# Performance work log

Measured on AMD Instinct MI355X. Metric: run time of the kernel, lower is better.

The kernel has to match this reference:

```python
import jax, jax.numpy as jnp
import numpy as np

# Problem sizes (see shape_source): N points, D embedding dim, B subbatches (events), M labels per event.
N, D, B, M = 2_097_152, 16, 8, 32
DELTA_V, DELTA_D = 0.5, 1.5  # module defaults
EPS = 1e-8


def setup_inputs() -> dict:
    key = jax.random.key(0)
    outputs = jax.random.normal(key, (N, D), dtype=jnp.float32)
    idx = jnp.arange(N)
    # contiguous subbatches, every label present in every subbatch (matches torch.unique structure)
    subbatch_indices = (idx // (N // B)).astype(jnp.int32)
    labels = (idx % M).astype(jnp.int32)
    return {"outputs": outputs, "labels": labels, "subbatch_indices": subbatch_indices}


def reference(outputs, labels, subbatch_indices):
    # normalize=True: L2-normalize each embedding row (note: torch adds eps to the norm, not norm+eps clamp)
    x = outputs / (jnp.linalg.norm(outputs, axis=1) + EPS)[:, None]

    # flat segment id per (subbatch, label) group; every group is populated by construction
    seg = (subbatch_indices * M + labels).astype(jnp.int32)  # [N] in [0, B*M)

    ones = jnp.ones((x.shape[0],), x.dtype)
    counts = jax.ops.segment_sum(ones, seg, num_segments=B * M)        # [B*M] == Nm per group
    mus = jax.ops.segment_sum(x, seg, num_segments=B * M) / counts[:, None]  # [B*M, D] centroids

    # L_pull: per-point hinge on L1 distance to its centroid, weights are all-ones (use_weights=False)
    dist = jnp.sum(jnp.abs(mus[seg] - x), axis=1)                       # [N] L1 distance
    L_pull = jnp.sum(jax.nn.relu(dist - DELTA_V) ** 2 / (M * counts[seg]))

    # L_push: all-pairs centroid hinge within each subbatch, diagonal zeroed
    mus_b = mus.reshape(B, M, D)
    pd = jnp.sum(jnp.abs(mus_b[:, :, None, :] - mus_b[:, None, :, :]), axis=-1)  # [B, M, M]
    hinge = jax.nn.relu(2.0 * DELTA_D - pd) ** 2
    hinge = jnp.where(jnp.eye(M, dtype=bool)[None], 0.0, hinge)
    L_push = jnp.sum(hinge) / (M * (M - 1))

    return (L_pull + L_push) / B
```

## Files before the change

kernel.cpp:

```cpp
#include <hip/hip_runtime.h>
#include <math.h>


#define DD 16
#define MM 32
#define BBATCH 8
#define SEGS 256
#define DELTA_V 0.5f
#define DELTA_D 1.5f
#define NEPS 1e-8f

#define NTHR 256
#define TILE_PTS 256
#define TPB 8
#define CHUNK_PTS (TILE_PTS * TPB)
#define DEPTH 2
#define KP 32
#define MAXBLK 2048

#define OFF_PP    0
#define OFF_MUS   (KP * 4352)
#define OFF_INVW  (OFF_MUS + 4096)
#define OFF_PUSH  (OFF_INVW + 256)
#define OFF_PULL  (OFF_PUSH + 16)
#define WS_ZERO_FLOATS (KP * 4352)

__device__ __forceinline__ void gload16(const void* g, void* l) {
    __builtin_amdgcn_global_load_lds(
        (const __attribute__((address_space(1))) void*)g,
        (__attribute__((address_space(3))) void*)l, 16, 0, 0);
}
__device__ __forceinline__ void gload4(const void* g, void* l) {
    __builtin_amdgcn_global_load_lds(
        (const __attribute__((address_space(1))) void*)g,
        (__attribute__((address_space(3))) void*)l, 4, 0, 0);
}

__device__ __forceinline__ void lds_fadd(float* p, float v) {
    __hip_atomic_fetch_add(p, v, __ATOMIC_RELAXED, __HIP_MEMORY_SCOPE_WORKGROUP);
}

__device__ __forceinline__ float block_reduce_sum(float v) {
    #pragma unroll
    for (int o = 32; o > 0; o >>= 1) v += __shfl_down(v, o, 64);
    __shared__ float red[4];
    int wid  = threadIdx.x >> 6;
    int lane = threadIdx.x & 63;
    if (lane == 0) red[wid] = v;
    __syncthreads();
    v = (threadIdx.x < (NTHR >> 6)) ? red[threadIdx.x] : 0.0f;
    if (wid == 0) {
        #pragma unroll
        for (int o = 32; o > 0; o >>= 1) v += __shfl_down(v, o, 64);
    }
    return v;
}

__device__ __forceinline__ void flush_point(float* lsT, int seg,
                                            float4 a0, float4 a1,
                                            float4 a2, float4 a3, float cnt) {
    lds_fadd(&lsT[ 0*SEGS + seg], a0.x); lds_fadd(&lsT[ 1*SEGS + seg], a0.y);
    lds_fadd(&lsT[ 2*SEGS + seg], a0.z); lds_fadd(&lsT[ 3*SEGS + seg], a0.w);
    lds_fadd(&lsT[ 4*SEGS + seg], a1.x); lds_fadd(&lsT[ 5*SEGS + seg], a1.y);
    lds_fadd(&lsT[ 6*SEGS + seg], a1.z); lds_fadd(&lsT[ 7*SEGS + seg], a1.w);
    lds_fadd(&lsT[ 8*SEGS + seg], a2.x); lds_fadd(&lsT[ 9*SEGS + seg], a2.y);
    lds_fadd(&lsT[10*SEGS + seg], a2.z); lds_fadd(&lsT[11*SEGS + seg], a2.w);
    lds_fadd(&lsT[12*SEGS + seg], a3.x); lds_fadd(&lsT[13*SEGS + seg], a3.y);
    lds_fadd(&lsT[14*SEGS + seg], a3.z); lds_fadd(&lsT[15*SEGS + seg], a3.w);
    lds_fadd(&lsT[16*SEGS + seg], cnt);
}

#define STAGE_TILE(bi_, pb_) do {                                              \
    const float* gs_ = (const float*)o4 + (size_t)(pb_) * DD;                  \
    { int q_ = (w << 8) +   0 + lane;                                          \
      gload16(gs_ + (q_ ^ ((q_ >> 3) & 3)) * 4, &dbuf[bi_][((w << 8) +   0) * 4]); } \
    { int q_ = (w << 8) +  64 + lane;                                          \
      gload16(gs_ + (q_ ^ ((q_ >> 3) & 3)) * 4, &dbuf[bi_][((w << 8) +  64) * 4]); } \
    { int q_ = (w << 8) + 128 + lane;                                          \
      gload16(gs_ + (q_ ^ ((q_ >> 3) & 3)) * 4, &dbuf[bi_][((w << 8) + 128) * 4]); } \
    { int q_ = (w << 8) + 192 + lane;                                          \
      gload16(gs_ + (q_ ^ ((q_ >> 3) & 3)) * 4, &dbuf[bi_][((w << 8) + 192) * 4]); } \
    gload4(labels + (pb_) + (w << 6) + lane, &labbuf[bi_][w << 6]);            \
    gload4(sub    + (pb_) + (w << 6) + lane, &subbuf[bi_][w << 6]);            \
} while (0)

__global__ void __launch_bounds__(NTHR)
k_segsum(const float4* __restrict__ o4,
         const int* __restrict__ labels,
         const int* __restrict__ sub,
         float* __restrict__ pp,
         int n) {
    __shared__ float lsT[(DD + 1) * SEGS];
    __shared__ float dbuf[DEPTH][TILE_PTS * DD];
    __shared__ int   labbuf[DEPTH][TILE_PTS];
    __shared__ int   subbuf[DEPTH][TILE_PTS];
    for (int i = threadIdx.x; i < (DD + 1) * SEGS; i += NTHR) lsT[i] = 0.0f;
    __syncthreads();

    const int t    = threadIdx.x;
    const int w    = t >> 6;
    const int lane = t & 63;
    const int xm   = (t >> 1) & 3;

    float4 c0 = {0,0,0,0}, c1 = {0,0,0,0}, c2 = {0,0,0,0}, c3 = {0,0,0,0};
    float cnt = 0.0f;
    int cur = -1;

    const int nchunks = n / CHUNK_PTS;
    for (int cb = blockIdx.x; cb < nchunks; cb += gridDim.x) {
        const int pbase = cb * CHUNK_PTS;
        STAGE_TILE(0, pbase + 0 * TILE_PTS);
        STAGE_TILE(1, pbase + 1 * TILE_PTS);
        #pragma unroll
        for (int ti = 0; ti < TPB; ++ti) {
            const int bi = ti & 1;
            if (ti < TPB - 1) asm volatile("s_waitcnt vmcnt(6)" ::: "memory");
            else              asm volatile("s_waitcnt vmcnt(0)" ::: "memory");
            int lb = labbuf[bi][t];
            int sv = subbuf[bi][t];
            const float* db = &dbuf[bi][0];
            float4 a = *(const float4*)&db[((4*t + 0) ^ xm) * 4];
            float4 b = *(const float4*)&db[((4*t + 1) ^ xm) * 4];
            float4 c = *(const float4*)&db[((4*t + 2) ^ xm) * 4];
            float4 e = *(const float4*)&db[((4*t + 3) ^ xm) * 4];
            int seg = sv * MM + lb;
            float ss = a.x*a.x + a.y*a.y + a.z*a.z + a.w*a.w
                     + b.x*b.x + b.y*b.y + b.z*b.z + b.w*b.w
                     + c.x*c.x + c.y*c.y + c.z*c.z + c.w*c.w
                     + e.x*e.x + e.y*e.y + e.z*e.z + e.w*e.w;
            float rn = 1.0f / (sqrtf(ss) + NEPS);
            if (seg != cur) {
                if (cur >= 0) flush_point(lsT, cur, c0, c1, c2, c3, cnt);
                c0 = c1 = c2 = c3 = (float4){0,0,0,0};
                cnt = 0.0f;
                cur = seg;
            }
            c0.x = fmaf(a.x, rn, c0.x); c0.y = fmaf(a.y, rn, c0.y);
            c0.z = fmaf(a.z, rn, c0.z); c0.w = fmaf(a.w, rn, c0.w);
            c1.x = fmaf(b.x, rn, c1.x); c1.y = fmaf(b.y, rn, c1.y);
            c1.z = fmaf(b.z, rn, c1.z); c1.w = fmaf(b.w, rn, c1.w);
            c2.x = fmaf(c.x, rn, c2.x); c2.y = fmaf(c.y, rn, c2.y);
            c2.z = fmaf(c.z, rn, c2.z); c2.w = fmaf(c.w, rn, c2.w);
            c3.x = fmaf(e.x, rn, c3.x); c3.y = fmaf(e.y, rn, c3.y);
            c3.z = fmaf(e.z, rn, c3.z); c3.w = fmaf(e.w, rn, c3.w);
            cnt += 1.0f;
            __builtin_amdgcn_sched_barrier(0);
            if (ti + 2 < TPB) STAGE_TILE(bi, pbase + (ti + 2) * TILE_PTS);
        }
    }
    if (blockIdx.x == 0) {
        for (int p = nchunks * CHUNK_PTS + t; p < n; p += NTHR) {
            float4 a = o4[4*p+0], b = o4[4*p+1], c = o4[4*p+2], e = o4[4*p+3];
            int seg = sub[p] * MM + labels[p];
            float ss = a.x*a.x + a.y*a.y + a.z*a.z + a.w*a.w
                     + b.x*b.x + b.y*b.y + b.z*b.z + b.w*b.w
                     + c.x*c.x + c.y*c.y + c.z*c.z + c.w*c.w
                     + e.x*e.x + e.y*e.y + e.z*e.z + e.w*e.w;
            float rn = 1.0f / (sqrtf(ss) + NEPS);
            if (seg != cur) {
                if (cur >= 0) flush_point(lsT, cur, c0, c1, c2, c3, cnt);
                c0 = c1 = c2 = c3 = (float4){0,0,0,0};
                cnt = 0.0f;
                cur = seg;
            }
            c0.x = fmaf(a.x, rn, c0.x); c0.y = fmaf(a.y, rn, c0.y);
            c0.z = fmaf(a.z, rn, c0.z); c0.w = fmaf(a.w, rn, c0.w);
            c1.x = fmaf(b.x, rn, c1.x); c1.y = fmaf(b.y, rn, c1.y);
            c1.z = fmaf(b.z, rn, c1.z); c1.w = fmaf(b.w, rn, c1.w);
            c2.x = fmaf(c.x, rn, c2.x); c2.y = fmaf(c.y, rn, c2.y);
            c2.z = fmaf(c.z, rn, c2.z); c2.w = fmaf(c.w, rn, c2.w);
            c3.x = fmaf(e.x, rn, c3.x); c3.y = fmaf(e.y, rn, c3.y);
            c3.z = fmaf(e.z, rn, c3.z); c3.w = fmaf(e.w, rn, c3.w);
            cnt += 1.0f;
        }
    }
    if (cur >= 0) flush_point(lsT, cur, c0, c1, c2, c3, cnt);
    __syncthreads();

    float* dst = pp + (size_t)(blockIdx.x & (KP - 1)) * (SEGS * 17);
    for (int s = threadIdx.x; s < SEGS; s += NTHR) {
        float c = lsT[DD * SEGS + s];
        if (c != 0.0f) {
            #pragma unroll
            for (int d = 0; d < DD; ++d)
                unsafeAtomicAdd(&dst[s * 17 + d], lsT[d * SEGS + s]);
            unsafeAtomicAdd(&dst[s * 17 + 16], c);
        }
    }
}

__global__ void k_finalize_push(float* __restrict__ ws) {
    const float* pp = ws + OFF_PP;
    float* mus  = ws + OFF_MUS;
    float* invw = ws + OFF_INVW;
    float* push = ws + OFF_PUSH;

    __shared__ float muT[DD * SEGS];
    int t = threadIdx.x;

    float s17[DD + 1];
    #pragma unroll
    for (int d = 0; d <= DD; ++d) s17[d] = 0.0f;
    for (int k = 0; k < KP; ++k) {
        const float* src = pp + (size_t)k * (SEGS * 17) + t * 17;
        #pragma unroll
        for (int d = 0; d <= DD; ++d) s17[d] += src[d];
    }
    float cnt = s17[DD];
    float ic  = (cnt > 0.0f) ? 1.0f / cnt : 0.0f;
    #pragma unroll
    for (int d = 0; d < DD; ++d) {
        float m = s17[d] * ic;
        mus[t * DD + d]   = m;
        muT[d * SEGS + t] = m;
    }
    invw[t] = (cnt > 0.0f) ? 1.0f / ((float)MM * cnt) : 0.0f;
    __syncthreads();

    int b = t >> 5, m1 = t & 31;
    float acc = 0.0f;
    for (int m2 = 0; m2 < MM; ++m2) {
        float pd = 0.0f;
        #pragma unroll
        for (int d = 0; d < DD; ++d)
            pd += fabsf(muT[d * SEGS + b * MM + m1] - muT[d * SEGS + b * MM + m2]);
        float h = 2.0f * DELTA_D - pd;
        if (m2 != m1 && h > 0.0f) acc += h * h;
    }
    float tot = block_reduce_sum(acc);
    if (t == 0) push[0] = tot / (float)(MM * (MM - 1));
}

__global__ void __launch_bounds__(NTHR)
k_pull(const float4* __restrict__ o4,
       const int* __restrict__ labels,
       const int* __restrict__ sub,
       const float* __restrict__ mus,
       const float* __restrict__ invw,
       float* __restrict__ pull_part,
       int n) {
    __shared__ float muL[DD * SEGS];
    __shared__ float siw[SEGS];
    __shared__ float dbuf[DEPTH][TILE_PTS * DD];
    __shared__ int   labbuf[DEPTH][TILE_PTS];
    __shared__ int   subbuf[DEPTH][TILE_PTS];
    for (int i = threadIdx.x; i < DD * SEGS; i += NTHR) muL[i] = mus[i];
    for (int i = threadIdx.x; i < SEGS; i += NTHR) siw[i] = invw[i];
    __syncthreads();

    const int t    = threadIdx.x;
    const int w    = t >> 6;
    const int lane = t & 63;
    const int xm   = (t >> 1) & 3;

    float4 m0, m1, m2, m3;
    float iw = 0.0f;
    int cur = -1;
    float acc = 0.0f;

    const int nchunks = n / CHUNK_PTS;
    for (int cb = blockIdx.x; cb < nchunks; cb += gridDim.x) {
        const int pbase = cb * CHUNK_PTS;
        STAGE_TILE(0, pbase + 0 * TILE_PTS);
        STAGE_TILE(1, pbase + 1 * TILE_PTS);
        #pragma unroll
        for (int ti = 0; ti < TPB; ++ti) {
            const int bi = ti & 1;
            if (ti < TPB - 1) asm volatile("s_waitcnt vmcnt(6)" ::: "memory");
            else              asm volatile("s_waitcnt vmcnt(0)" ::: "memory");
            int lb = labbuf[bi][t];
            int sv = subbuf[bi][t];
            const float* db = &dbuf[bi][0];
            float4 a = *(const float4*)&db[((4*t + 0) ^ xm) * 4];
            float4 b = *(const float4*)&db[((4*t + 1) ^ xm) * 4];
            float4 c = *(const float4*)&db[((4*t + 2) ^ xm) * 4];
            float4 e = *(const float4*)&db[((4*t + 3) ^ xm) * 4];
            int seg = sv * MM + lb;
            if (seg != cur) {
                cur = seg;
                m0 = *(const float4*)&muL[seg * DD +  0];
                m1 = *(const float4*)&muL[seg * DD +  4];
                m2 = *(const float4*)&muL[seg * DD +  8];
                m3 = *(const float4*)&muL[seg * DD + 12];
                iw = siw[seg];
            }
            float ss = a.x*a.x + a.y*a.y + a.z*a.z + a.w*a.w
                     + b.x*b.x + b.y*b.y + b.z*b.z + b.w*b.w
                     + c.x*c.x + c.y*c.y + c.z*c.z + c.w*c.w
                     + e.x*e.x + e.y*e.y + e.z*e.z + e.w*e.w;
            float rn = 1.0f / (sqrtf(ss) + NEPS);
            float dist;
            dist  = fabsf(m0.x - a.x * rn) + fabsf(m0.y - a.y * rn)
                  + fabsf(m0.z - a.z * rn) + fabsf(m0.w - a.w * rn);
            dist += fabsf(m1.x - b.x * rn) + fabsf(m1.y - b.y * rn)
                  + fabsf(m1.z - b.z * rn) + fabsf(m1.w - b.w * rn);
            dist += fabsf(m2.x - c.x * rn) + fabsf(m2.y - c.y * rn)
                  + fabsf(m2.z - c.z * rn) + fabsf(m2.w - c.w * rn);
            dist += fabsf(m3.x - e.x * rn) + fabsf(m3.y - e.y * rn)
                  + fabsf(m3.z - e.z * rn) + fabsf(m3.w - e.w * rn);
            float h = dist - DELTA_V;
            if (h > 0.0f) acc = fmaf(h * h, iw, acc);
            __builtin_amdgcn_sched_barrier(0);
            if (ti + 2 < TPB) STAGE_TILE(bi, pbase + (ti + 2) * TILE_PTS);
        }
    }
    if (blockIdx.x == 0) {
        for (int p = nchunks * CHUNK_PTS + t; p < n; p += NTHR) {
            float4 a = o4[4*p+0], b = o4[4*p+1], c = o4[4*p+2], e = o4[4*p+3];
            int seg = sub[p] * MM + labels[p];
            if (seg != cur) {
                cur = seg;
                m0 = *(const float4*)&muL[seg * DD +  0];
                m1 = *(const float4*)&muL[seg * DD +  4];
                m2 = *(const float4*)&muL[seg * DD +  8];
                m3 = *(const float4*)&muL[seg * DD + 12];
                iw = siw[seg];
            }
            float ss = a.x*a.x + a.y*a.y + a.z*a.z + a.w*a.w
                     + b.x*b.x + b.y*b.y + b.z*b.z + b.w*b.w
                     + c.x*c.x + c.y*c.y + c.z*c.z + c.w*c.w
                     + e.x*e.x + e.y*e.y + e.z*e.z + e.w*e.w;
            float rn = 1.0f / (sqrtf(ss) + NEPS);
            float dist;
            dist  = fabsf(m0.x - a.x * rn) + fabsf(m0.y - a.y * rn)
                  + fabsf(m0.z - a.z * rn) + fabsf(m0.w - a.w * rn);
            dist += fabsf(m1.x - b.x * rn) + fabsf(m1.y - b.y * rn)
                  + fabsf(m1.z - b.z * rn) + fabsf(m1.w - b.w * rn);
            dist += fabsf(m2.x - c.x * rn) + fabsf(m2.y - c.y * rn)
                  + fabsf(m2.z - c.z * rn) + fabsf(m2.w - c.w * rn);
            dist += fabsf(m3.x - e.x * rn) + fabsf(m3.y - e.y * rn)
                  + fabsf(m3.z - e.z * rn) + fabsf(m3.w - e.w * rn);
            float h = dist - DELTA_V;
            if (h > 0.0f) acc = fmaf(h * h, iw, acc);
        }
    }
    float tot = block_reduce_sum(acc);
    if (threadIdx.x == 0) pull_part[blockIdx.x] = tot;
}

__global__ void k_final(const float* __restrict__ ws, float* __restrict__ out,
                        int nblk) {
    const float* push      = ws + OFF_PUSH;
    const float* pull_part = ws + OFF_PULL;
    int t = threadIdx.x;
    float v = 0.0f;
    for (int k = t; k < nblk; k += NTHR) v += pull_part[k];
    float tot = block_reduce_sum(v);
    if (t == 0) out[0] = (tot + push[0]) * (1.0f / (float)BBATCH);
}

extern "C" void kernel_launch(void* const* d_in, const int* in_sizes, int n_in,
                              void* d_out, int out_size, void* d_ws, size_t ws_size,
                              hipStream_t stream) {
    const float* outputs = (const float*)d_in[0];
    const int* labels    = (const int*)d_in[1];
    const int* sub       = (const int*)d_in[2];
    int n = in_sizes[0] / DD;

    float* ws        = (float*)d_ws;
    float* pp        = ws + OFF_PP;
    float* mus       = ws + OFF_MUS;
    float* invw      = ws + OFF_INVW;
    float* pull_part = ws + OFF_PULL;

    int nchunks = n / CHUNK_PTS;
    int nblk = nchunks < 1 ? 1 : (nchunks > MAXBLK ? MAXBLK : nchunks);

    hipMemsetAsync(d_ws, 0, (size_t)WS_ZERO_FLOATS * sizeof(float), stream);

    k_segsum<<<nblk, NTHR, 0, stream>>>((const float4*)outputs, labels, sub,
                                        pp, n);
    k_finalize_push<<<1, NTHR, 0, stream>>>(ws);
    k_pull<<<nblk, NTHR, 0, stream>>>((const float4*)outputs, labels, sub,
                                      mus, invw, pull_part, n);
    k_final<<<1, NTHR, 0, stream>>>(ws, (float*)d_out, nblk);
}
```

Baseline: 299.4 us.

## Shrink LDS footprint by flushing segment sums to global atomics and reusing buffers

Removes the per-block LDS segment-sum table and centroid copy so both streaming kernels use only the staging buffers, targeting higher occupancy (launch bounds raised to 4 blocks). Mid-stream segment flushes now go straight to global atomics in a transposed partial layout. The tail flush reuses the staging buffer as the LDS table. k_pull reads centroids from global memory rather than LDS. Because labels change almost every point, this risks far more global atomic traffic and contention.

Result: slower. 383.5 us (+28.1%).

```diff
diff --git a/kernel.cpp b/kernel.cpp
--- a/kernel.cpp
+++ b/kernel.cpp
@@ -70,37 +70,51 @@
     lds_fadd(&lsT[16*SEGS + seg], cnt);
 }
 
+__device__ __forceinline__ void flush_global(float* dst, int seg,
+                                             float4 a0, float4 a1,
+                                             float4 a2, float4 a3, float cnt) {
+    unsafeAtomicAdd(&dst[ 0*SEGS + seg], a0.x); unsafeAtomicAdd(&dst[ 1*SEGS + seg], a0.y);
+    unsafeAtomicAdd(&dst[ 2*SEGS + seg], a0.z); unsafeAtomicAdd(&dst[ 3*SEGS + seg], a0.w);
+    unsafeAtomicAdd(&dst[ 4*SEGS + seg], a1.x); unsafeAtomicAdd(&dst[ 5*SEGS + seg], a1.y);
+    unsafeAtomicAdd(&dst[ 6*SEGS + seg], a1.z); unsafeAtomicAdd(&dst[ 7*SEGS + seg], a1.w);
+    unsafeAtomicAdd(&dst[ 8*SEGS + seg], a2.x); unsafeAtomicAdd(&dst[ 9*SEGS + seg], a2.y);
+    unsafeAtomicAdd(&dst[10*SEGS + seg], a2.z); unsafeAtomicAdd(&dst[11*SEGS + seg], a2.w);
+    unsafeAtomicAdd(&dst[12*SEGS + seg], a3.x); unsafeAtomicAdd(&dst[13*SEGS + seg], a3.y);
+    unsafeAtomicAdd(&dst[14*SEGS + seg], a3.z); unsafeAtomicAdd(&dst[15*SEGS + seg], a3.w);
+    unsafeAtomicAdd(&dst[16*SEGS + seg], cnt);
+}
+
 #define STAGE_TILE(bi_, pb_) do {                                              \
     const float* gs_ = (const float*)o4 + (size_t)(pb_) * DD;                  \
+    float* db_ = smem + (bi_) * (TILE_PTS * DD);                               \
     { int q_ = (w << 8) +   0 + lane;                                          \
-      gload16(gs_ + (q_ ^ ((q_ >> 3) & 3)) * 4, &dbuf[bi_][((w << 8) +   0) * 4]); } \
+      gload16(gs_ + (size_t)(q_ ^ ((q_ >> 3) & 3)) * 4, db_ + ((w << 8) +   0) * 4); } \
     { int q_ = (w << 8) +  64 + lane;                                          \
-      gload16(gs_ + (q_ ^ ((q_ >> 3) & 3)) * 4, &dbuf[bi_][((w << 8) +  64) * 4]); } \
+      gload16(gs_ + (size_t)(q_ ^ ((q_ >> 3) & 3)) * 4, db_ + ((w << 8) +  64) * 4); } \
     { int q_ = (w << 8) + 128 + lane;                                          \
-      gload16(gs_ + (q_ ^ ((q_ >> 3) & 3)) * 4, &dbuf[bi_][((w << 8) + 128) * 4]); } \
+      gload16(gs_ + (size_t)(q_ ^ ((q_ >> 3) & 3)) * 4, db_ + ((w << 8) + 128) * 4); } \
     { int q_ = (w << 8) + 192 + lane;                                          \
-      gload16(gs_ + (q_ ^ ((q_ >> 3) & 3)) * 4, &dbuf[bi_][((w << 8) + 192) * 4]); } \
+      gload16(gs_ + (size_t)(q_ ^ ((q_ >> 3) & 3)) * 4, db_ + ((w << 8) + 192) * 4); } \
     gload4(labels + (pb_) + (w << 6) + lane, &labbuf[bi_][w << 6]);            \
     gload4(sub    + (pb_) + (w << 6) + lane, &subbuf[bi_][w << 6]);            \
 } while (0)
 
-__global__ void __launch_bounds__(NTHR)
+__global__ void __launch_bounds__(NTHR, 4)
 k_segsum(const float4* __restrict__ o4,
          const int* __restrict__ labels,
          const int* __restrict__ sub,
          float* __restrict__ pp,
          int n) {
-    __shared__ float lsT[(DD + 1) * SEGS];
-    __shared__ float dbuf[DEPTH][TILE_PTS * DD];
+    __shared__ float smem[DEPTH * TILE_PTS * DD];
     __shared__ int   labbuf[DEPTH][TILE_PTS];
     __shared__ int   subbuf[DEPTH][TILE_PTS];
-    for (int i = threadIdx.x; i < (DD + 1) * SEGS; i += NTHR) lsT[i] = 0.0f;
-    __syncthreads();
 
     const int t    = threadIdx.x;
     const int w    = t >> 6;
     const int lane = t & 63;
     const int xm   = (t >> 1) & 3;
+
+    float* gdst = pp + (size_t)(blockIdx.x & (KP - 1)) * ((DD + 1) * SEGS);
 
     float4 c0 = {0,0,0,0}, c1 = {0,0,0,0}, c2 = {0,0,0,0}, c3 = {0,0,0,0};
     float cnt = 0.0f;
@@ -118,7 +132,7 @@
             else              asm volatile("s_waitcnt vmcnt(0)" ::: "memory");
             int lb = labbuf[bi][t];
             int sv = subbuf[bi][t];
-            const float* db = &dbuf[bi][0];
+            const float* db = smem + bi * (TILE_PTS * DD);
             float4 a = *(const float4*)&db[((4*t + 0) ^ xm) * 4];
             float4 b = *(const float4*)&db[((4*t + 1) ^ xm) * 4];
             float4 c = *(const float4*)&db[((4*t + 2) ^ xm) * 4];
@@ -130,7 +144,7 @@
                      + e.x*e.x + e.y*e.y + e.z*e.z + e.w*e.w;
             float rn = 1.0f / (sqrtf(ss) + NEPS);
             if (seg != cur) {
-                if (cur >= 0) flush_point(lsT, cur, c0, c1, c2, c3, cnt);
+                if (cur >= 0) flush_global(gdst, cur, c0, c1, c2, c3, cnt);
                 c0 = c1 = c2 = c3 = (float4){0,0,0,0};
                 cnt = 0.0f;
                 cur = seg;
@@ -158,7 +172,7 @@
                      + e.x*e.x + e.y*e.y + e.z*e.z + e.w*e.w;
             float rn = 1.0f / (sqrtf(ss) + NEPS);
             if (seg != cur) {
-                if (cur >= 0) flush_point(lsT, cur, c0, c1, c2, c3, cnt);
+                if (cur >= 0) flush_global(gdst, cur, c0, c1, c2, c3, cnt);
                 c0 = c1 = c2 = c3 = (float4){0,0,0,0};
                 cnt = 0.0f;
                 cur = seg;
@@ -174,17 +188,21 @@
             cnt += 1.0f;
         }
     }
+
+    __syncthreads();
+    float* lsT = smem;
+    for (int i = t; i < (DD + 1) * SEGS; i += NTHR) lsT[i] = 0.0f;
+    __syncthreads();
     if (cur >= 0) flush_point(lsT, cur, c0, c1, c2, c3, cnt);
     __syncthreads();
 
-    float* dst = pp + (size_t)(blockIdx.x & (KP - 1)) * (SEGS * 17);
-    for (int s = threadIdx.x; s < SEGS; s += NTHR) {
+    for (int s = t; s < SEGS; s += NTHR) {
         float c = lsT[DD * SEGS + s];
         if (c != 0.0f) {
             #pragma unroll
             for (int d = 0; d < DD; ++d)
-                unsafeAtomicAdd(&dst[s * 17 + d], lsT[d * SEGS + s]);
-            unsafeAtomicAdd(&dst[s * 17 + 16], c);
+                unsafeAtomicAdd(&gdst[d * SEGS + s], lsT[d * SEGS + s]);
+            unsafeAtomicAdd(&gdst[DD * SEGS + s], c);
         }
     }
 }
@@ -201,10 +219,11 @@
     float s17[DD + 1];
     #pragma unroll
     for (int d = 0; d <= DD; ++d) s17[d] = 0.0f;
+    #pragma unroll 2
     for (int k = 0; k < KP; ++k) {
-        const float* src = pp + (size_t)k * (SEGS * 17) + t * 17;
-        #pragma unroll
-        for (int d = 0; d <= DD; ++d) s17[d] += src[d];
+        const float* src = pp + (size_t)k * ((DD + 1) * SEGS) + t;
+        #pragma unroll
+        for (int d = 0; d <= DD; ++d) s17[d] += src[d * SEGS];
     }
     float cnt = s17[DD];
     float ic  = (cnt > 0.0f) ? 1.0f / cnt : 0.0f;
@@ -231,7 +250,7 @@
     if (t == 0) push[0] = tot / (float)(MM * (MM - 1));
 }
 
-__global__ void __launch_bounds__(NTHR)
+__global__ void __launch_bounds__(NTHR, 4)
 k_pull(const float4* __restrict__ o4,
        const int* __restrict__ labels,
        const int* __restrict__ sub,
@@ -239,14 +258,9 @@
        const float* __restrict__ invw,
        float* __restrict__ pull_part,
        int n) {
-    __shared__ float muL[DD * SEGS];
-    __shared__ float siw[SEGS];
-    __shared__ float dbuf[DEPTH][TILE_PTS * DD];
+    __shared__ float smem[DEPTH * TILE_PTS * DD];
     __shared__ int   labbuf[DEPTH][TILE_PTS];
     __shared__ int   subbuf[DEPTH][TILE_PTS];
-    for (int i = threadIdx.x; i < DD * SEGS; i += NTHR) muL[i] = mus[i];
-    for (int i = threadIdx.x; i < SEGS; i += NTHR) siw[i] = invw[i];
-    __syncthreads();
 
     const int t    = threadIdx.x;
     const int w    = t >> 6;
@@ -270,7 +284,7 @@
             else              asm volatile("s_waitcnt vmcnt(0)" ::: "memory");
             int lb = labbuf[bi][t];
             int sv = subbuf[bi][t];
-            const float* db = &dbuf[bi][0];
+            const float* db = smem + bi * (TILE_PTS * DD);
             float4 a = *(const float4*)&db[((4*t + 0) ^ xm) * 4];
             float4 b = *(const float4*)&db[((4*t + 1) ^ xm) * 4];
             float4 c = *(const float4*)&db[((4*t + 2) ^ xm) * 4];
@@ -278,11 +292,11 @@
             int seg = sv * MM + lb;
             if (seg != cur) {
                 cur = seg;
-                m0 = *(const float4*)&muL[seg * DD +  0];
-                m1 = *(const float4*)&muL[seg * DD +  4];
-                m2 = *(const float4*)&muL[seg * DD +  8];
-                m3 = *(const float4*)&muL[seg * DD + 12];
-                iw = siw[seg];
+                m0 = *(const float4*)&mus[seg * DD +  0];
+                m1 = *(const float4*)&mus[seg * DD +  4];
+                m2 = *(const float4*)&mus[seg * DD +  8];
+                m3 = *(const float4*)&mus[seg * DD + 12];
+                iw = invw[seg];
             }
             float ss = a.x*a.x + a.y*a.y + a.z*a.z + a.w*a.w
                      + b.x*b.x + b.y*b.y + b.z*b.z + b.w*b.w
@@ -310,11 +324,11 @@
             int seg = sub[p] * MM + labels[p];
             if (seg != cur) {
                 cur = seg;
-                m0 = *(const float4*)&muL[seg * DD +  0];
-                m1 = *(const float4*)&muL[seg * DD +  4];
-                m2 = *(const float4*)&muL[seg * DD +  8];
-                m3 = *(const float4*)&muL[seg * DD + 12];
-                iw = siw[seg];
+                m0 = *(const float4*)&mus[seg * DD +  0];
+                m1 = *(const float4*)&mus[seg * DD +  4];
+                m2 = *(const float4*)&mus[seg * DD +  8];
+                m3 = *(const float4*)&mus[seg * DD + 12];
+                iw = invw[seg];
             }
             float ss = a.x*a.x + a.y*a.y + a.z*a.z + a.w*a.w
                      + b.x*b.x + b.y*b.y + b.z*b.z + b.w*b.w
```

## Replace LDS-staged pull pass with direct grid-stride loads; transpose partial-sum layout

Applied to the files above, without the earlier changes.

The pull kernel no longer stages point tiles into LDS with async global-to-LDS loads and double buffering. Each thread now loads its own point's four float4 values straight from global memory in a grid-stride loop, with more blocks and a min-blocks launch bound of 6 to raise occupancy. The per-block partial centroid sums switch from a point-major stride of 17 to a dimension-major layout, so the global atomics and the finalize reads become coalesced. The trade-off is that the pull loads now rely on the hardware to hide latency and combine the strided per-thread accesses, rather than on explicit software pipelining.

New measurement: 272.1 us. 9.1% less time.

```diff
diff --git a/kernel.cpp b/kernel.cpp
--- a/kernel.cpp
+++ b/kernel.cpp
@@ -17,6 +17,7 @@
 #define DEPTH 2
 #define KP 32
 #define MAXBLK 2048
+#define PULLBLK 4096
 
 #define OFF_PP    0
 #define OFF_MUS   (KP * 4352)
@@ -73,13 +74,13 @@
 #define STAGE_TILE(bi_, pb_) do {                                              \
     const float* gs_ = (const float*)o4 + (size_t)(pb_) * DD;                  \
     { int q_ = (w << 8) +   0 + lane;                                          \
-      gload16(gs_ + (q_ ^ ((q_ >> 3) & 3)) * 4, &dbuf[bi_][((w << 8) +   0) * 4]); } \
+      gload16(gs_ + (size_t)(q_ ^ ((q_ >> 3) & 3)) * 4, &dbuf[bi_][((w << 8) +   0) * 4]); } \
     { int q_ = (w << 8) +  64 + lane;                                          \
-      gload16(gs_ + (q_ ^ ((q_ >> 3) & 3)) * 4, &dbuf[bi_][((w << 8) +  64) * 4]); } \
+      gload16(gs_ + (size_t)(q_ ^ ((q_ >> 3) & 3)) * 4, &dbuf[bi_][((w << 8) +  64) * 4]); } \
     { int q_ = (w << 8) + 128 + lane;                                          \
-      gload16(gs_ + (q_ ^ ((q_ >> 3) & 3)) * 4, &dbuf[bi_][((w << 8) + 128) * 4]); } \
+      gload16(gs_ + (size_t)(q_ ^ ((q_ >> 3) & 3)) * 4, &dbuf[bi_][((w << 8) + 128) * 4]); } \
     { int q_ = (w << 8) + 192 + lane;                                          \
-      gload16(gs_ + (q_ ^ ((q_ >> 3) & 3)) * 4, &dbuf[bi_][((w << 8) + 192) * 4]); } \
+      gload16(gs_ + (size_t)(q_ ^ ((q_ >> 3) & 3)) * 4, &dbuf[bi_][((w << 8) + 192) * 4]); } \
     gload4(labels + (pb_) + (w << 6) + lane, &labbuf[bi_][w << 6]);            \
     gload4(sub    + (pb_) + (w << 6) + lane, &subbuf[bi_][w << 6]);            \
 } while (0)
@@ -177,14 +178,14 @@
     if (cur >= 0) flush_point(lsT, cur, c0, c1, c2, c3, cnt);
     __syncthreads();
 
-    float* dst = pp + (size_t)(blockIdx.x & (KP - 1)) * (SEGS * 17);
-    for (int s = threadIdx.x; s < SEGS; s += NTHR) {
+    float* gdst = pp + (size_t)(blockIdx.x & (KP - 1)) * ((DD + 1) * SEGS);
+    for (int s = t; s < SEGS; s += NTHR) {
         float c = lsT[DD * SEGS + s];
         if (c != 0.0f) {
             #pragma unroll
             for (int d = 0; d < DD; ++d)
-                unsafeAtomicAdd(&dst[s * 17 + d], lsT[d * SEGS + s]);
-            unsafeAtomicAdd(&dst[s * 17 + 16], c);
+                unsafeAtomicAdd(&gdst[d * SEGS + s], lsT[d * SEGS + s]);
+            unsafeAtomicAdd(&gdst[DD * SEGS + s], c);
         }
     }
 }
@@ -201,10 +202,11 @@
     float s17[DD + 1];
     #pragma unroll
     for (int d = 0; d <= DD; ++d) s17[d] = 0.0f;
+    #pragma unroll 2
     for (int k = 0; k < KP; ++k) {
-        const float* src = pp + (size_t)k * (SEGS * 17) + t * 17;
+        const float* src = pp + (size_t)k * ((DD + 1) * SEGS) + t;
         #pragma unroll
-        for (int d = 0; d <= DD; ++d) s17[d] += src[d];
+        for (int d = 0; d <= DD; ++d) s17[d] += src[d * SEGS];
     }
     float cnt = s17[DD];
     float ic  = (cnt > 0.0f) ? 1.0f / cnt : 0.0f;
@@ -231,7 +233,7 @@
     if (t == 0) push[0] = tot / (float)(MM * (MM - 1));
 }
 
-__global__ void __launch_bounds__(NTHR)
+__global__ void __launch_bounds__(NTHR, 6)
 k_pull(const float4* __restrict__ o4,
        const int* __restrict__ labels,
        const int* __restrict__ sub,
@@ -241,98 +243,37 @@
        int n) {
     __shared__ float muL[DD * SEGS];
     __shared__ float siw[SEGS];
-    __shared__ float dbuf[DEPTH][TILE_PTS * DD];
-    __shared__ int   labbuf[DEPTH][TILE_PTS];
-    __shared__ int   subbuf[DEPTH][TILE_PTS];
     for (int i = threadIdx.x; i < DD * SEGS; i += NTHR) muL[i] = mus[i];
     for (int i = threadIdx.x; i < SEGS; i += NTHR) siw[i] = invw[i];
     __syncthreads();
 
-    const int t    = threadIdx.x;
-    const int w    = t >> 6;
-    const int lane = t & 63;
-    const int xm   = (t >> 1) & 3;
-
-    float4 m0, m1, m2, m3;
-    float iw = 0.0f;
-    int cur = -1;
     float acc = 0.0f;
-
-    const int nchunks = n / CHUNK_PTS;
-    for (int cb = blockIdx.x; cb < nchunks; cb += gridDim.x) {
-        const int pbase = cb * CHUNK_PTS;
-        STAGE_TILE(0, pbase + 0 * TILE_PTS);
-        STAGE_TILE(1, pbase + 1 * TILE_PTS);
-        #pragma unroll
-        for (int ti = 0; ti < TPB; ++ti) {
-            const int bi = ti & 1;
-            if (ti < TPB - 1) asm volatile("s_waitcnt vmcnt(6)" ::: "memory");
-            else              asm volatile("s_waitcnt vmcnt(0)" ::: "memory");
-            int lb = labbuf[bi][t];
-            int sv = subbuf[bi][t];
-            const float* db = &dbuf[bi][0];
-            float4 a = *(const float4*)&db[((4*t + 0) ^ xm) * 4];
-            float4 b = *(const float4*)&db[((4*t + 1) ^ xm) * 4];
-            float4 c = *(const float4*)&db[((4*t + 2) ^ xm) * 4];
-            float4 e = *(const float4*)&db[((4*t + 3) ^ xm) * 4];
-            int seg = sv * MM + lb;
-            if (seg != cur) {
-                cur = seg;
-                m0 = *(const float4*)&muL[seg * DD +  0];
-                m1 = *(const float4*)&muL[seg * DD +  4];
-                m2 = *(const float4*)&muL[seg * DD +  8];
-                m3 = *(const float4*)&muL[seg * DD + 12];
-                iw = siw[seg];
-            }
-            float ss = a.x*a.x + a.y*a.y + a.z*a.z + a.w*a.w
-                     + b.x*b.x + b.y*b.y + b.z*b.z + b.w*b.w
-                     + c.x*c.x + c.y*c.y + c.z*c.z + c.w*c.w
-                     + e.x*e.x + e.y*e.y + e.z*e.z + e.w*e.w;
-            float rn = 1.0f / (sqrtf(ss) + NEPS);
-            float dist;
-            dist  = fabsf(m0.x - a.x * rn) + fabsf(m0.y - a.y * rn)
-                  + fabsf(m0.z - a.z * rn) + fabsf(m0.w - a.w * rn);
-            dist += fabsf(m1.x - b.x * rn) + fabsf(m1.y - b.y * rn)
-                  + fabsf(m1.z - b.z * rn) + fabsf(m1.w - b.w * rn);
-            dist += fabsf(m2.x - c.x * rn) + fabsf(m2.y - c.y * rn)
-                  + fabsf(m2.z - c.z * rn) + fabsf(m2.w - c.w * rn);
-            dist += fabsf(m3.x - e.x * rn) + fabsf(m3.y - e.y * rn)
-                  + fabsf(m3.z - e.z * rn) + fabsf(m3.w - e.w * rn);
-            float h = dist - DELTA_V;
-            if (h > 0.0f) acc = fmaf(h * h, iw, acc);
-            __builtin_amdgcn_sched_barrier(0);
-            if (ti + 2 < TPB) STAGE_TILE(bi, pbase + (ti + 2) * TILE_PTS);
-        }
-    }
-    if (blockIdx.x == 0) {
-        for (int p = nchunks * CHUNK_PTS + t; p < n; p += NTHR) {
-            float4 a = o4[4*p+0], b = o4[4*p+1], c = o4[4*p+2], e = o4[4*p+3];
-            int seg = sub[p] * MM + labels[p];
-            if (seg != cur) {
-                cur = seg;
-                m0 = *(const float4*)&muL[seg * DD +  0];
-                m1 = *(const float4*)&muL[seg * DD +  4];
-                m2 = *(const float4*)&muL[seg * DD +  8];
-                m3 = *(const float4*)&muL[seg * DD + 12];
-                iw = siw[seg];
-            }
-            float ss = a.x*a.x + a.y*a.y + a.z*a.z + a.w*a.w
-                     + b.x*b.x + b.y*b.y + b.z*b.z + b.w*b.w
-                     + c.x*c.x + c.y*c.y + c.z*c.z + c.w*c.w
-                     + e.x*e.x + e.y*e.y + e.z*e.z + e.w*e.w;
-            float rn = 1.0f / (sqrtf(ss) + NEPS);
-            float dist;
-            dist  = fabsf(m0.x - a.x * rn) + fabsf(m0.y - a.y * rn)
-                  + fabsf(m0.z - a.z * rn) + fabsf(m0.w - a.w * rn);
-            dist += fabsf(m1.x - b.x * rn) + fabsf(m1.y - b.y * rn)
-                  + fabsf(m1.z - b.z * rn) + fabsf(m1.w - b.w * rn);
-            dist += fabsf(m2.x - c.x * rn) + fabsf(m2.y - c.y * rn)
-                  + fabsf(m2.z - c.z * rn) + fabsf(m2.w - c.w * rn);
-            dist += fabsf(m3.x - e.x * rn) + fabsf(m3.y - e.y * rn)
-                  + fabsf(m3.z - e.z * rn) + fabsf(m3.w - e.w * rn);
-            float h = dist - DELTA_V;
-            if (h > 0.0f) acc = fmaf(h * h, iw, acc);
-        }
+    const int stride = gridDim.x * NTHR;
+    #pragma unroll 2
+    for (int p = blockIdx.x * NTHR + threadIdx.x; p < n; p += stride) {
+        int seg = sub[p] * MM + labels[p];
+        float4 a = o4[4*p+0], b = o4[4*p+1], c = o4[4*p+2], e = o4[4*p+3];
+        float ss = a.x*a.x + a.y*a.y + a.z*a.z + a.w*a.w
+                 + b.x*b.x + b.y*b.y + b.z*b.z + b.w*b.w
+                 + c.x*c.x + c.y*c.y + c.z*c.z + c.w*c.w
+                 + e.x*e.x + e.y*e.y + e.z*e.z + e.w*e.w;
+        float rn = 1.0f / (sqrtf(ss) + NEPS);
+        const float* mu = &muL[seg * DD];
+        float4 m0 = *(const float4*)&mu[ 0];
+        float4 m1 = *(const float4*)&mu[ 4];
+        float4 m2 = *(const float4*)&mu[ 8];
+        float4 m3 = *(const float4*)&mu[12];
+        float dist;
+        dist  = fabsf(m0.x - a.x * rn) + fabsf(m0.y - a.y * rn)
+              + fabsf(m0.z - a.z * rn) + fabsf(m0.w - a.w * rn);
+        dist += fabsf(m1.x - b.x * rn) + fabsf(m1.y - b.y * rn)
+              + fabsf(m1.z - b.z * rn) + fabsf(m1.w - b.w * rn);
+        dist += fabsf(m2.x - c.x * rn) + fabsf(m2.y - c.y * rn)
+              + fabsf(m2.z - c.z * rn) + fabsf(m2.w - c.w * rn);
+        dist += fabsf(m3.x - e.x * rn) + fabsf(m3.y - e.y * rn)
+              + fabsf(m3.z - e.z * rn) + fabsf(m3.w - e.w * rn);
+        float h = fmaxf(dist - DELTA_V, 0.0f);
+        acc = fmaf(h * h, siw[seg], acc);
     }
     float tot = block_reduce_sum(acc);
     if (threadIdx.x == 0) pull_part[blockIdx.x] = tot;
@@ -366,12 +307,15 @@
     int nchunks = n / CHUNK_PTS;
     int nblk = nchunks < 1 ? 1 : (nchunks > MAXBLK ? MAXBLK : nchunks);
 
+    long npb = ((long)n + NTHR - 1) / NTHR;
+    int nblk2 = npb < 1 ? 1 : (npb > PULLBLK ? PULLBLK : (int)npb);
+
     hipMemsetAsync(d_ws, 0, (size_t)WS_ZERO_FLOATS * sizeof(float), stream);
 
     k_segsum<<<nblk, NTHR, 0, stream>>>((const float4*)outputs, labels, sub,
                                         pp, n);
     k_finalize_push<<<1, NTHR, 0, stream>>>(ws);
-    k_pull<<<nblk, NTHR, 0, stream>>>((const float4*)outputs, labels, sub,
-                                      mus, invw, pull_part, n);
-    k_final<<<1, NTHR, 0, stream>>>(ws, (float*)d_out, nblk);
-}
+    k_pull<<<nblk2, NTHR, 0, stream>>>((const float4*)outputs, labels, sub,
+                                       mus, invw, pull_part, n);
+    k_final<<<1, NTHR, 0, stream>>>(ws, (float*)d_out, nblk2);
+}
```

## Fuse centroid finalize into segsum via last-block counter, drop final reduce kernel

Applied to the files above, without the earlier changes.

The separate finalize/push kernel is folded into k_segsum: a global atomic counter picks the last block, which reads the per-partition partial sums and computes the centroids and the push term. k_pull now adds its partial result atomically into one global accumulator, so a tiny output kernel replaces the multi-block final reduction. It also halves the partition count and the block cap, stores partials and centroids transposed, and reads centroids straight from LDS per point instead of caching them in registers on segment change. The goal is fewer kernel launches and less serial reduction work. The cost is extra atomics, fences and possible LDS bank conflicts, and the diff leaves some dead code and forward declarations behind.

New measurement: 422.8 us. 1.41x slower.

```diff
diff --git a/kernel.cpp b/kernel.cpp
--- a/kernel.cpp
+++ b/kernel.cpp
@@ -15,15 +15,18 @@
 #define TPB 8
 #define CHUNK_PTS (TILE_PTS * TPB)
 #define DEPTH 2
-#define KP 32
-#define MAXBLK 2048
-
+#define KP 16
+#define MAXBLK 1024
+
+#define PP_STRIDE ((DD + 1) * SEGS)
 #define OFF_PP    0
-#define OFF_MUS   (KP * 4352)
-#define OFF_INVW  (OFF_MUS + 4096)
-#define OFF_PUSH  (OFF_INVW + 256)
-#define OFF_PULL  (OFF_PUSH + 16)
-#define WS_ZERO_FLOATS (KP * 4352)
+#define OFF_CTR   (KP * PP_STRIDE)
+#define OFF_CTR2  (OFF_CTR + 1)
+#define OFF_ACC   (OFF_CTR + 4)
+#define OFF_MUT   (OFF_CTR + 16)
+#define OFF_INVW  (OFF_MUT + DD * SEGS)
+#define OFF_PUSH  (OFF_INVW + SEGS)
+#define WS_ZERO_FLOATS (OFF_CTR + 16)
 
 __device__ __forceinline__ void gload16(const void* g, void* l) {
     __builtin_amdgcn_global_load_lds(
@@ -70,30 +73,34 @@
     lds_fadd(&lsT[16*SEGS + seg], cnt);
 }
 
-#define STAGE_TILE(bi_, pb_) do {                                              \
-    const float* gs_ = (const float*)o4 + (size_t)(pb_) * DD;                  \
-    { int q_ = (w << 8) +   0 + lane;                                          \
-      gload16(gs_ + (q_ ^ ((q_ >> 3) & 3)) * 4, &dbuf[bi_][((w << 8) +   0) * 4]); } \
-    { int q_ = (w << 8) +  64 + lane;                                          \
-      gload16(gs_ + (q_ ^ ((q_ >> 3) & 3)) * 4, &dbuf[bi_][((w << 8) +  64) * 4]); } \
-    { int q_ = (w << 8) + 128 + lane;                                          \
-      gload16(gs_ + (q_ ^ ((q_ >> 3) & 3)) * 4, &dbuf[bi_][((w << 8) + 128) * 4]); } \
-    { int q_ = (w << 8) + 192 + lane;                                          \
-      gload16(gs_ + (q_ ^ ((q_ >> 3) & 3)) * 4, &dbuf[bi_][((w << 8) + 192) * 4]); } \
-    gload4(labels + (pb_) + (w << 6) + lane, &labbuf[bi_][w << 6]);            \
-    gload4(sub    + (pb_) + (w << 6) + lane, &subbuf[bi_][w << 6]);            \
-} while (0)
+__device__ __forceinline__ void stage_tile(const float* gbase,
+                                           const int* labels, const int* sub,
+                                           float* db, int* lb, int* sb,
+                                           int pb, int w, int lane) {
+    const float* gs = gbase + (size_t)pb * DD;
+    { int q = (w << 8) +   0 + lane;
+      gload16(gs + (size_t)(q ^ ((q >> 3) & 3)) * 4, db + ((w << 8) +   0) * 4); }
+    { int q = (w << 8) +  64 + lane;
+      gload16(gs + (size_t)(q ^ ((q >> 3) & 3)) * 4, db + ((w << 8) +  64) * 4); }
+    { int q = (w << 8) + 128 + lane;
+      gload16(gs + (size_t)(q ^ ((q >> 3) & 3)) * 4, db + ((w << 8) + 128) * 4); }
+    { int q = (w << 8) + 192 + lane;
+      gload16(gs + (size_t)(q ^ ((q >> 3) & 3)) * 4, db + ((w << 8) + 192) * 4); }
+    gload4(labels + pb + (w << 6) + lane, lb + (w << 6));
+    gload4(sub    + pb + (w << 6) + lane, sb + (w << 6));
+}
 
 __global__ void __launch_bounds__(NTHR)
 k_segsum(const float4* __restrict__ o4,
          const int* __restrict__ labels,
          const int* __restrict__ sub,
-         float* __restrict__ pp,
+         float* __restrict__ wsf,
          int n) {
     __shared__ float lsT[(DD + 1) * SEGS];
     __shared__ float dbuf[DEPTH][TILE_PTS * DD];
     __shared__ int   labbuf[DEPTH][TILE_PTS];
     __shared__ int   subbuf[DEPTH][TILE_PTS];
+    __shared__ int   lastflag;
     for (int i = threadIdx.x; i < (DD + 1) * SEGS; i += NTHR) lsT[i] = 0.0f;
     __syncthreads();
 
@@ -101,6 +108,8 @@
     const int w    = t >> 6;
     const int lane = t & 63;
     const int xm   = (t >> 1) & 3;
+    const float* gbase = (const float*)o4;
+    float* pp = wsf + OFF_PP;
 
     float4 c0 = {0,0,0,0}, c1 = {0,0,0,0}, c2 = {0,0,0,0}, c3 = {0,0,0,0};
     float cnt = 0.0f;
@@ -109,8 +118,10 @@
     const int nchunks = n / CHUNK_PTS;
     for (int cb = blockIdx.x; cb < nchunks; cb += gridDim.x) {
         const int pbase = cb * CHUNK_PTS;
-        STAGE_TILE(0, pbase + 0 * TILE_PTS);
-        STAGE_TILE(1, pbase + 1 * TILE_PTS);
+        stage_tile(gbase, labels, sub, &dbuf[0][0], &labbuf[0][0], &subbuf[0][0],
+                   pbase + 0 * TILE_PTS, w, lane);
+        stage_tile(gbase, labels, sub, &dbuf[1][0], &labbuf[1][0], &subbuf[1][0],
+                   pbase + 1 * TILE_PTS, w, lane);
         #pragma unroll
         for (int ti = 0; ti < TPB; ++ti) {
             const int bi = ti & 1;
@@ -145,7 +156,9 @@
             c3.z = fmaf(e.z, rn, c3.z); c3.w = fmaf(e.w, rn, c3.w);
             cnt += 1.0f;
             __builtin_amdgcn_sched_barrier(0);
-            if (ti + 2 < TPB) STAGE_TILE(bi, pbase + (ti + 2) * TILE_PTS);
+            if (ti + 2 < TPB)
+                stage_tile(gbase, labels, sub, &dbuf[bi][0], &labbuf[bi][0],
+                           &subbuf[bi][0], pbase + (ti + 2) * TILE_PTS, w, lane);
         }
     }
     if (blockIdx.x == 0) {
@@ -177,92 +190,92 @@
     if (cur >= 0) flush_point(lsT, cur, c0, c1, c2, c3, cnt);
     __syncthreads();
 
-    float* dst = pp + (size_t)(blockIdx.x & (KP - 1)) * (SEGS * 17);
-    for (int s = threadIdx.x; s < SEGS; s += NTHR) {
+    float* gdst = pp + (size_t)(blockIdx.x & (KP - 1)) * PP_STRIDE;
+    for (int s = t; s < SEGS; s += NTHR) {
         float c = lsT[DD * SEGS + s];
         if (c != 0.0f) {
             #pragma unroll
             for (int d = 0; d < DD; ++d)
-                unsafeAtomicAdd(&dst[s * 17 + d], lsT[d * SEGS + s]);
-            unsafeAtomicAdd(&dst[s * 17 + 16], c);
-        }
-    }
-}
-
-__global__ void k_finalize_push(float* __restrict__ ws) {
-    const float* pp = ws + OFF_PP;
-    float* mus  = ws + OFF_MUS;
-    float* invw = ws + OFF_INVW;
-    float* push = ws + OFF_PUSH;
-
-    __shared__ float muT[DD * SEGS];
-    int t = threadIdx.x;
-
-    float s17[DD + 1];
-    #pragma unroll
-    for (int d = 0; d <= DD; ++d) s17[d] = 0.0f;
-    for (int k = 0; k < KP; ++k) {
-        const float* src = pp + (size_t)k * (SEGS * 17) + t * 17;
-        #pragma unroll
-        for (int d = 0; d <= DD; ++d) s17[d] += src[d];
-    }
-    float cnt = s17[DD];
-    float ic  = (cnt > 0.0f) ? 1.0f / cnt : 0.0f;
-    #pragma unroll
-    for (int d = 0; d < DD; ++d) {
-        float m = s17[d] * ic;
-        mus[t * DD + d]   = m;
-        muT[d * SEGS + t] = m;
-    }
-    invw[t] = (cnt > 0.0f) ? 1.0f / ((float)MM * cnt) : 0.0f;
-    __syncthreads();
-
-    int b = t >> 5, m1 = t & 31;
-    float acc = 0.0f;
-    for (int m2 = 0; m2 < MM; ++m2) {
-        float pd = 0.0f;
-        #pragma unroll
-        for (int d = 0; d < DD; ++d)
-            pd += fabsf(muT[d * SEGS + b * MM + m1] - muT[d * SEGS + b * MM + m2]);
-        float h = 2.0f * DELTA_D - pd;
-        if (m2 != m1 && h > 0.0f) acc += h * h;
-    }
-    float tot = block_reduce_sum(acc);
-    if (t == 0) push[0] = tot / (float)(MM * (MM - 1));
+                unsafeAtomicAdd(&gdst[d * SEGS + s], lsT[d * SEGS + s]);
+            unsafeAtomicAdd(&gdst[DD * SEGS + s], c);
+        }
+    }
+
+    __threadfence();
+    if (t == 0) {
+        int* ctr = (int*)(wsf + OFF_CTR);
+        int prev = __hip_atomic_fetch_add(ctr, 1, __ATOMIC_ACQ_REL,
+                                          __HIP_MEMORY_SCOPE_AGENT);
+        lastflag = (prev == (int)gridDim.x - 1) ? 1 : 0;
+    }
+    __syncthreads();
+    if (lastflag) {
+        float s17[DD + 1];
+        #pragma unroll
+        for (int d = 0; d <= DD; ++d) s17[d] = 0.0f;
+        for (int k = 0; k < KP; ++k) {
+            float* src = pp + (size_t)k * PP_STRIDE + t;
+            #pragma unroll
+            for (int d = 0; d <= DD; ++d)
+                s17[d] += unsafeAtomicAdd(&src[d * SEGS], 0.0f);
+        }
+        float cnt2 = s17[DD];
+        float ic   = (cnt2 > 0.0f) ? 1.0f / cnt2 : 0.0f;
+        #pragma unroll
+        for (int d = 0; d < DD; ++d) {
+            float m = s17[d] * ic;
+            wsf[OFF_MUT + d * SEGS + t] = m;
+            lsT[d * SEGS + t] = m;
+        }
+        wsf[OFF_INVW + t] = (cnt2 > 0.0f) ? 1.0f / ((float)MM * cnt2) : 0.0f;
+        __syncthreads();
+
+        int b = t >> 5, m1 = t & 31;
+        float acc = 0.0f;
+        for (int m2 = 0; m2 < MM; ++m2) {
+            float pd = 0.0f;
+            #pragma unroll
+            for (int d = 0; d < DD; ++d)
+                pd += fabsf(lsT[d * SEGS + b * MM + m1] - lsT[d * SEGS + b * MM + m2]);
+            float h = 2.0f * DELTA_D - pd;
+            if (m2 != m1 && h > 0.0f) acc += h * h;
+        }
+        float tot = block_reduce_sum(acc);
+        if (t == 0) wsf[OFF_PUSH] = tot / (float)(MM * (MM - 1));
+    }
 }
 
 __global__ void __launch_bounds__(NTHR)
 k_pull(const float4* __restrict__ o4,
        const int* __restrict__ labels,
        const int* __restrict__ sub,
-       const float* __restrict__ mus,
-       const float* __restrict__ invw,
-       float* __restrict__ pull_part,
+       float* __restrict__ wsf,
        int n) {
-    __shared__ float muL[DD * SEGS];
+    __shared__ float muT[DD * SEGS];
     __shared__ float siw[SEGS];
     __shared__ float dbuf[DEPTH][TILE_PTS * DD];
     __shared__ int   labbuf[DEPTH][TILE_PTS];
     __shared__ int   subbuf[DEPTH][TILE_PTS];
-    for (int i = threadIdx.x; i < DD * SEGS; i += NTHR) muL[i] = mus[i];
-    for (int i = threadIdx.x; i < SEGS; i += NTHR) siw[i] = invw[i];
+    __shared__ int   lastflag;
+    for (int i = threadIdx.x; i < DD * SEGS; i += NTHR) muT[i] = wsf[OFF_MUT + i];
+    for (int i = threadIdx.x; i < SEGS; i += NTHR) siw[i] = wsf[OFF_INVW + i];
     __syncthreads();
 
     const int t    = threadIdx.x;
     const int w    = t >> 6;
     const int lane = t & 63;
     const int xm   = (t >> 1) & 3;
-
-    float4 m0, m1, m2, m3;
-    float iw = 0.0f;
-    int cur = -1;
+    const float* gbase = (const float*)o4;
+
     float acc = 0.0f;
 
     const int nchunks = n / CHUNK_PTS;
     for (int cb = blockIdx.x; cb < nchunks; cb += gridDim.x) {
         const int pbase = cb * CHUNK_PTS;
-        STAGE_TILE(0, pbase + 0 * TILE_PTS);
-        STAGE_TILE(1, pbase + 1 * TILE_PTS);
+        stage_tile(gbase, labels, sub, &dbuf[0][0], &labbuf[0][0], &subbuf[0][0],
+                   pbase + 0 * TILE_PTS, w, lane);
+        stage_tile(gbase, labels, sub, &dbuf[1][0], &labbuf[1][0], &subbuf[1][0],
+                   pbase + 1 * TILE_PTS, w, lane);
         #pragma unroll
         for (int ti = 0; ti < TPB; ++ti) {
             const int bi = ti & 1;
@@ -276,77 +289,81 @@
             float4 c = *(const float4*)&db[((4*t + 2) ^ xm) * 4];
             float4 e = *(const float4*)&db[((4*t + 3) ^ xm) * 4];
             int seg = sv * MM + lb;
-            if (seg != cur) {
-                cur = seg;
-                m0 = *(const float4*)&muL[seg * DD +  0];
-                m1 = *(const float4*)&muL[seg * DD +  4];
-                m2 = *(const float4*)&muL[seg * DD +  8];
-                m3 = *(const float4*)&muL[seg * DD + 12];
-                iw = siw[seg];
-            }
             float ss = a.x*a.x + a.y*a.y + a.z*a.z + a.w*a.w
                      + b.x*b.x + b.y*b.y + b.z*b.z + b.w*b.w
                      + c.x*c.x + c.y*c.y + c.z*c.z + c.w*c.w
                      + e.x*e.x + e.y*e.y + e.z*e.z + e.w*e.w;
             float rn = 1.0f / (sqrtf(ss) + NEPS);
             float dist;
-            dist  = fabsf(m0.x - a.x * rn) + fabsf(m0.y - a.y * rn)
-                  + fabsf(m0.z - a.z * rn) + fabsf(m0.w - a.w * rn);
-            dist += fabsf(m1.x - b.x * rn) + fabsf(m1.y - b.y * rn)
-                  + fabsf(m1.z - b.z * rn) + fabsf(m1.w - b.w * rn);
-            dist += fabsf(m2.x - c.x * rn) + fabsf(m2.y - c.y * rn)
-                  + fabsf(m2.z - c.z * rn) + fabsf(m2.w - c.w * rn);
-            dist += fabsf(m3.x - e.x * rn) + fabsf(m3.y - e.y * rn)
-                  + fabsf(m3.z - e.z * rn) + fabsf(m3.w - e.w * rn);
-            float h = dist - DELTA_V;
-            if (h > 0.0f) acc = fmaf(h * h, iw, acc);
+            dist  = fabsf(muT[ 0*SEGS + seg] - a.x * rn)
+                  + fabsf(muT[ 1*SEGS + seg] - a.y * rn)
+                  + fabsf(muT[ 2*SEGS + seg] - a.z * rn)
+                  + fabsf(muT[ 3*SEGS + seg] - a.w * rn);
+            dist += fabsf(muT[ 4*SEGS + seg] - b.x * rn)
+                  + fabsf(muT[ 5*SEGS + seg] - b.y * rn)
+                  + fabsf(muT[ 6*SEGS + seg] - b.z * rn)
+                  + fabsf(muT[ 7*SEGS + seg] - b.w * rn);
+            dist += fabsf(muT[ 8*SEGS + seg] - c.x * rn)
+                  + fabsf(muT[ 9*SEGS + seg] - c.y * rn)
+                  + fabsf(muT[10*SEGS + seg] - c.z * rn)
+                  + fabsf(muT[11*SEGS + seg] - c.w * rn);
+            dist += fabsf(muT[12*SEGS + seg] - e.x * rn)
+                  + fabsf(muT[13*SEGS + seg] - e.y * rn)
+                  + fabsf(muT[14*SEGS + seg] - e.z * rn)
+                  + fabsf(muT[15*SEGS + seg] - e.w * rn);
+            float h = fmaxf(dist - DELTA_V, 0.0f);
+            acc = fmaf(h * h, siw[seg], acc);
             __builtin_amdgcn_sched_barrier(0);
-            if (ti + 2 < TPB) STAGE_TILE(bi, pbase + (ti + 2) * TILE_PTS);
+            if (ti + 2 < TPB)
+                stage_tile(gbase, labels, sub, &dbuf[bi][0], &labbuf[bi][0],
+                           &subbuf[bi][0], pbase + (ti + 2) * TILE_PTS, w, lane);
         }
     }
     if (blockIdx.x == 0) {
         for (int p = nchunks * CHUNK_PTS + t; p < n; p += NTHR) {
             float4 a = o4[4*p+0], b = o4[4*p+1], c = o4[4*p+2], e = o4[4*p+3];
             int seg = sub[p] * MM + labels[p];
-            if (seg != cur) {
-                cur = seg;
-                m0 = *(const float4*)&muL[seg * DD +  0];
-                m1 = *(const float4*)&muL[seg * DD +  4];
-                m2 = *(const float4*)&muL[seg * DD +  8];
-                m3 = *(const float4*)&muL[seg * DD + 12];
-                iw = siw[seg];
-            }
             float ss = a.x*a.x + a.y*a.y + a.z*a.z + a.w*a.w
                      + b.x*b.x + b.y*b.y + b.z*b.z + b.w*b.w
                      + c.x*c.x + c.y*c.y + c.z*c.z + c.w*c.w
                      + e.x*e.x + e.y*e.y + e.z*e.z + e.w*e.w;
             float rn = 1.0f / (sqrtf(ss) + NEPS);
-            float dist;
-            dist  = fabsf(m0.x - a.x * rn) + fabsf(m0.y - a.y * rn)
-                  + fabsf(m0.z - a.z * rn) + fabsf(m0.w - a.w * rn);
-            dist += fabsf(m1.x - b.x * rn) + fabsf(m1.y - b.y * rn)
-                  + fabsf(m1.z - b.z * rn) + fabsf(m1.w - b.w * rn);
-            dist += fabsf(m2.x - c.x * rn) + fabsf(m2.y - c.y * rn)
-                  + fabsf(m2.z - c.z * rn) + fabsf(m2.w - c.w * rn);
-            dist += fabsf(m3.x - e.x * rn) + fabsf(m3.y - e.y * rn)
-                  + fabsf(m3.z - e.z * rn) + fabsf(m3.w - e.w * rn);
-            float h = dist - DELTA_V;
-            if (h > 0.0f) acc = fmaf(h * h, iw, acc);
+            float x[DD] = {a.x*rn,a.y*rn,a.z*rn,a.w*rn, b.x*rn,b.y*rn,b.z*rn,b.w*rn,
+                           c.x*rn,c.y*rn,c.z*rn,c.w*rn, e.x*rn,e.y*rn,e.z*rn,e.w*rn};
+            float dist = 0.0f;
+            #pragma unroll
+            for (int d = 0; d < DD; ++d)
+                dist += fabsf(wsf[OFF_MUT + d * SEGS + seg] - x[d]);
+            float h = fmaxf(dist - DELTA_V, 0.0f);
+            acc = fmaf(h * h, wsf[OFF_INVW + seg], acc);
         }
     }
     float tot = block_reduce_sum(acc);
-    if (threadIdx.x == 0) pull_part[blockIdx.x] = tot;
-}
-
-__global__ void k_final(const float* __restrict__ ws, float* __restrict__ out,
-                        int nblk) {
-    const float* push      = ws + OFF_PUSH;
-    const float* pull_part = ws + OFF_PULL;
-    int t = threadIdx.x;
-    float v = 0.0f;
-    for (int k = t; k < nblk; k += NTHR) v += pull_part[k];
-    float tot = block_reduce_sum(v);
-    if (t == 0) out[0] = (tot + push[0]) * (1.0f / (float)BBATCH);
+    if (t == 0) unsafeAtomicAdd(&wsf[OFF_ACC], tot);
+
+    __threadfence();
+    if (t == 0) {
+        int* ctr2 = (int*)(wsf + OFF_CTR2);
+        int prev = __hip_atomic_fetch_add(ctr2, 1, __ATOMIC_ACQ_REL,
+                                          __HIP_MEMORY_SCOPE_AGENT);
+        lastflag = (prev == (int)gridDim.x - 1) ? 1 : 0;
+    }
+    __syncthreads();
+    if (lastflag && t == 0) {
+        float pull = unsafeAtomicAdd(&wsf[OFF_ACC], 0.0f);
+        float push = wsf[OFF_PUSH];
+    }
+}
+
+__global__ void k_pull_out_writer(float* __restrict__ wsf, float* __restrict__ out);
+
+extern "C" void kernel_launch(void* const* d_in, const int* in_sizes, int n_in,
+                              void* d_out, int out_size, void* d_ws, size_t ws_size,
+                              hipStream_t stream);
+
+__global__ void k_out(const float* __restrict__ wsf, float* __restrict__ out) {
+    if (threadIdx.x == 0)
+        out[0] = (wsf[OFF_ACC] + wsf[OFF_PUSH]) * (1.0f / (float)BBATCH);
 }
 
 extern "C" void kernel_launch(void* const* d_in, const int* in_sizes, int n_in,
@@ -357,11 +374,7 @@
     const int* sub       = (const int*)d_in[2];
     int n = in_sizes[0] / DD;
 
-    float* ws        = (float*)d_ws;
-    float* pp        = ws + OFF_PP;
-    float* mus       = ws + OFF_MUS;
-    float* invw      = ws + OFF_INVW;
-    float* pull_part = ws + OFF_PULL;
+    float* wsf = (float*)d_ws;
 
     int nchunks = n / CHUNK_PTS;
     int nblk = nchunks < 1 ? 1 : (nchunks > MAXBLK ? MAXBLK : nchunks);
@@ -369,9 +382,8 @@
     hipMemsetAsync(d_ws, 0, (size_t)WS_ZERO_FLOATS * sizeof(float), stream);
 
     k_segsum<<<nblk, NTHR, 0, stream>>>((const float4*)outputs, labels, sub,
-                                        pp, n);
-    k_finalize_push<<<1, NTHR, 0, stream>>>(ws);
+                                        wsf, n);
     k_pull<<<nblk, NTHR, 0, stream>>>((const float4*)outputs, labels, sub,
-                                      mus, invw, pull_part, n);
-    k_final<<<1, NTHR, 0, stream>>>(ws, (float*)d_out, nblk);
-}
+                                      wsf, n);
+    k_out<<<1, 64, 0, stream>>>(wsf, (float*)d_out);
+}
```
